# Optimization experiments

Measured on AMD Instinct MI355X. Metric: run time of the kernel, lower is better.

The kernel has to match this reference:

```python
import jax, jax.numpy as jnp
import numpy as np

N_NODES = 100000
N_EDGES = 1200000
IN_CH = 64
HID = 16
OUT_CH = 64
EDGE_DIM = 3


def _glorot(key, shape):
    fan_in, fan_out = shape[0], shape[1]
    lim = float(np.sqrt(6.0 / (fan_in + fan_out)))
    return jax.random.uniform(key, shape, jnp.float32, -lim, lim)


def setup_inputs() -> dict:
    key = jax.random.key(0)
    ks = jax.random.split(key, 16)
    x = jax.random.normal(ks[0], (N_NODES, IN_CH), jnp.float32)
    edge_index = jax.random.randint(ks[1], (2, N_EDGES), 0, N_NODES, jnp.int64)
    edge_attr = jax.random.normal(ks[2], (N_EDGES, EDGE_DIM), jnp.float32)
    return {
        "x": x,
        "edge_index": edge_index,
        "edge_attr": edge_attr,
        # conv1: in->16
        "W1l": _glorot(ks[3], (IN_CH, HID)), "b1l": jnp.zeros((HID,), jnp.float32),
        "W1r": _glorot(ks[4], (IN_CH, HID)), "b1r": jnp.zeros((HID,), jnp.float32),
        "W1e": _glorot(ks[5], (EDGE_DIM, IN_CH)), "b1e": jnp.zeros((IN_CH,), jnp.float32),
        # conv2: 16->out
        "W2l": _glorot(ks[6], (HID, OUT_CH)), "b2l": jnp.zeros((OUT_CH,), jnp.float32),
        "W2r": _glorot(ks[7], (HID, OUT_CH)), "b2r": jnp.zeros((OUT_CH,), jnp.float32),
        "W2e": _glorot(ks[8], (EDGE_DIM, HID)), "b2e": jnp.zeros((HID,), jnp.float32),
    }


def _sage_conv(x, src, dst, edge_attr, We, be, Wl, bl, Wr, br):
    # message: neighbor feature + projected edge attribute (edge_dim-aware SAGE)
    msg = x[src] + edge_attr @ We + be                       # [E, C_in]
    agg = jax.ops.segment_sum(msg, dst, num_segments=N_NODES)  # [N, C_in]
    deg = jax.ops.segment_sum(jnp.ones((msg.shape[0],), msg.dtype), dst,
                              num_segments=N_NODES)
    agg = agg / jnp.maximum(deg, 1.0)[:, None]               # mean aggregation
    return agg @ Wl + bl + x @ Wr + br                       # neighbor + self paths


def reference(x, edge_index, edge_attr,
              W1l, b1l, W1r, b1r, W1e, b1e,
              W2l, b2l, W2r, b2r, W2e, b2e):
    src, dst = edge_index[0], edge_index[1]
    h = jax.nn.relu(_sage_conv(x, src, dst, edge_attr, W1e, b1e, W1l, b1l, W1r, b1r))
    # F.dropout(training=self.training): eval mode -> identity
    out = _sage_conv(h, src, dst, edge_attr, W2e, b2e, W2l, b2l, W2r, b2r)
    return out
```

## Files before the change

kernel.cpp:

```cpp
#include <hip/hip_runtime.h>
#include <hip/hip_bf16.h>
#include <stdint.h>

#define N_NODES 100000
#define N_EDGES 1200000
#define IN_CH 64
#define HID 16
#define OUT_CH 64

#define BN 100
#define NB 1000
#define CAP 2048
#define SC_EPB 4096
#define SC_TPB 512
#define SC_EPT (SC_EPB / SC_TPB)

typedef __hip_bfloat16 bf16;

__device__ __forceinline__ float b2f(bf16 v) { return __bfloat162float(v); }
__device__ __forceinline__ float lo_f(uint32_t p) { return __uint_as_float(p << 16); }
__device__ __forceinline__ float hi_f(uint32_t p) { return __uint_as_float(p & 0xffff0000u); }
__device__ __forceinline__ uint16_t f2bb(float v) {
    bf16 h = __float2bfloat16(v);
    return *reinterpret_cast<uint16_t*>(&h);
}

__device__ __forceinline__ float loadf(const void* p, size_t i, int bf) {
    return bf ? b2f(((const bf16*)p)[i]) : ((const float*)p)[i];
}
__device__ __forceinline__ uint32_t bfbits(const void* p, size_t i, int bf) {
    if (bf) return ((const uint16_t*)p)[i];
    return f2bb(((const float*)p)[i]);
}
__device__ __forceinline__ int ld_dst(const int* p, int j, int i64) {
    if (i64) return ((const int2*)p)[(size_t)N_EDGES + j].x;
    return p[(size_t)N_EDGES + j];
}
__device__ __forceinline__ int ld_src(const int* p, int j, int i64) {
    if (i64) return ((const int2*)p)[j].x;
    return p[j];
}

__global__ void k_prep(const void* __restrict__ x, const int* __restrict__ ei,
                       const void* __restrict__ W1e, const void* __restrict__ b1e,
                       const void* __restrict__ W1l, float* __restrict__ wc,
                       int* __restrict__ flags) {
    __shared__ int s_bf;
    if (threadIdx.x == 0) {
        const uint16_t* u = (const uint16_t*)x;
        int cnt = 0;
        for (int i = 0; i < 64; ++i) {
            int e = (u[i] >> 7) & 0xff;
            cnt += (e >= 100 && e <= 140);
        }
        int bf = (cnt >= 50);
        const uint32_t* w = (const uint32_t*)ei;
        int z = 0;
        for (int i = 1; i < 64; i += 2) z += (w[i] == 0u);
        flags[0] = bf;
        flags[1] = (z >= 16);
        s_bf = bf;
    }
    __syncthreads();
    int bf = s_bf;
    int j = threadIdx.x;
    if (j >= HID) return;
    for (int r = 0; r < 3; ++r) {
        float s = 0.f;
        for (int k = 0; k < IN_CH; ++k)
            s += loadf(W1e, r * IN_CH + k, bf) * loadf(W1l, k * HID + j, bf);
        wc[r * HID + j] = s;
    }
    float s = 0.f;
    for (int k = 0; k < IN_CH; ++k)
        s += loadf(b1e, k, bf) * loadf(W1l, k * HID + j, bf);
    wc[3 * HID + j] = s;
}

__global__ void __launch_bounds__(256) k_y(const void* __restrict__ x,
                                           const void* __restrict__ W1l,
                                           const void* __restrict__ W1r,
                                           const void* __restrict__ b1l,
                                           const void* __restrict__ b1r,
                                           const int* __restrict__ flags,
                                           bf16* __restrict__ y,
                                           bf16* __restrict__ zh) {
    __shared__ float w[IN_CH * 32];
    __shared__ float bz[HID];
    int bf = flags[0];
    for (int t = threadIdx.x; t < IN_CH * 32; t += 256) {
        int k = t >> 5, cc = t & 31;
        w[t] = (cc < 16) ? loadf(W1l, k * HID + cc, bf) : loadf(W1r, k * HID + (cc - 16), bf);
    }
    if (threadIdx.x < HID)
        bz[threadIdx.x] = loadf(b1l, threadIdx.x, bf) + loadf(b1r, threadIdx.x, bf);
    __syncthreads();
    int tid = blockIdx.x * 256 + threadIdx.x;
    int row = tid >> 1;
    if (row >= N_NODES) return;
    int half = tid & 1, cs = half * 16;
    float acc[16];
#pragma unroll
    for (int j = 0; j < 16; ++j) acc[j] = 0.f;
    if (bf) {
        const uint4* xr = (const uint4*)((const uint16_t*)x + (size_t)row * IN_CH);
        uint4 q[8];
#pragma unroll
        for (int i = 0; i < 8; ++i) q[i] = xr[i];
        const uint32_t* qq = (const uint32_t*)q;
#pragma unroll
        for (int k2 = 0; k2 < 32; ++k2) {
            uint32_t u = qq[k2];
            float x0 = lo_f(u), x1 = hi_f(u);
            const float* w0 = &w[(2 * k2) * 32 + cs];
            const float* w1 = w0 + 32;
#pragma unroll
            for (int j = 0; j < 16; ++j) acc[j] += x0 * w0[j] + x1 * w1[j];
        }
    } else {
        const float4* xr = (const float4*)((const float*)x + (size_t)row * IN_CH);
#pragma unroll
        for (int c = 0; c < 4; ++c) {
            float4 f[4];
#pragma unroll
            for (int i = 0; i < 4; ++i) f[i] = xr[c * 4 + i];
            const float* ff = (const float*)f;
#pragma unroll
            for (int kk = 0; kk < 16; ++kk) {
                float xk = ff[kk];
                const float* wr = &w[(c * 16 + kk) * 32 + cs];
#pragma unroll
                for (int j = 0; j < 16; ++j) acc[j] += xk * wr[j];
            }
        }
    }
    if (half) {
#pragma unroll
        for (int j = 0; j < 16; ++j) acc[j] += bz[j];
    }
    uint32_t pk[8];
#pragma unroll
    for (int j2 = 0; j2 < 8; ++j2)
        pk[j2] = (uint32_t)f2bb(acc[2 * j2]) | ((uint32_t)f2bb(acc[2 * j2 + 1]) << 16);
    bf16* dst = half ? (zh + (size_t)row * HID) : (y + (size_t)row * HID);
    uint4* d4 = (uint4*)dst;
    d4[0] = make_uint4(pk[0], pk[1], pk[2], pk[3]);
    d4[1] = make_uint4(pk[4], pk[5], pk[6], pk[7]);
}

__global__ void __launch_bounds__(256) k_bhist(const int* __restrict__ ei,
                                               const int* __restrict__ flags,
                                               int* __restrict__ bcount) {
    __shared__ int lh[NB];
    for (int t = threadIdx.x; t < NB; t += 256) lh[t] = 0;
    __syncthreads();
    int i64 = flags[1];
    int stride = gridDim.x * 256;
    for (int e = blockIdx.x * 256 + threadIdx.x; e < N_EDGES; e += stride) {
        uint32_t dst = (uint32_t)ld_dst(ei, e, i64);
        atomicAdd(&lh[dst / BN], 1);
    }
    __syncthreads();
    for (int t = threadIdx.x; t < NB; t += 256)
        if (lh[t]) atomicAdd(&bcount[t], lh[t]);
}

__global__ void __launch_bounds__(1024) k_bscan(const int* __restrict__ bcount,
                                                int* __restrict__ boff,
                                                int* __restrict__ cursor) {
    __shared__ int s[1024];
    int t = threadIdx.x;
    int own = (t < NB) ? bcount[t] : 0;
    s[t] = own;
    __syncthreads();
    for (int off = 1; off < 1024; off <<= 1) {
        int v = (t >= off) ? s[t - off] : 0;
        __syncthreads();
        s[t] += v;
        __syncthreads();
    }
    if (t < NB) {
        int ex = s[t] - own;
        boff[t] = ex;
        cursor[t] = ex;
        if (t == NB - 1) boff[NB] = s[t];
    }
}

__global__ void __launch_bounds__(SC_TPB) k_bscatter(const int* __restrict__ ei,
                                                     const void* __restrict__ ea,
                                                     const int* __restrict__ flags,
                                                     int* __restrict__ cursor,
                                                     uint2* __restrict__ slots,
                                                     uint16_t* __restrict__ ea2v) {
    __shared__ int lhist[NB];
    __shared__ int lscan[NB];
    __shared__ int ldelta[NB];
    __shared__ int wsum[8];
    __shared__ uint2 lval[SC_EPB];
    __shared__ uint16_t lea[SC_EPB];
    __shared__ uint16_t lbid[SC_EPB];
    int t = threadIdx.x;
    for (int i = t; i < NB; i += SC_TPB) lhist[i] = 0;
    __syncthreads();
    int i64 = flags[1], bf = flags[0];
    int base = blockIdx.x * SC_EPB;
    uint32_t rb[SC_EPT], srcv[SC_EPT], ea01v[SC_EPT], ea2r[SC_EPT];
#pragma unroll
    for (int i = 0; i < SC_EPT; ++i) {
        int e = base + i * SC_TPB + t;
        rb[i] = 0xFFFFFFFFu;
        if (e < N_EDGES) {
            uint32_t d = (uint32_t)ld_dst(ei, e, i64);
            srcv[i] = (uint32_t)ld_src(ei, e, i64);
            ea01v[i] = bfbits(ea, (size_t)e * 3, bf) |
                       (bfbits(ea, (size_t)e * 3 + 1, bf) << 16);
            ea2r[i] = bfbits(ea, (size_t)e * 3 + 2, bf);
            uint32_t b = d / BN;
            uint32_t dl = d - b * BN;
            uint32_t r = (uint32_t)atomicAdd(&lhist[b], 1);
            rb[i] = (b << 19) | (dl << 12) | r;
        }
    }
    __syncthreads();
    int b0 = 2 * t, b1 = 2 * t + 1;
    int cnt0 = (b0 < NB) ? lhist[b0] : 0;
    int cnt1 = (b1 < NB) ? lhist[b1] : 0;
    int s_local = cnt0 + cnt1;
    int incl = s_local;
    int lane = t & 63;
#pragma unroll
    for (int d = 1; d < 64; d <<= 1) {
        int v = __shfl_up(incl, d);
        if (lane >= d) incl += v;
    }
    int w = t >> 6;
    if (lane == 63) wsum[w] = incl;
    __syncthreads();
    int wbase = 0, nst = 0;
#pragma unroll
    for (int i = 0; i < 8; ++i) {
        int v = wsum[i];
        wbase += (i < w) ? v : 0;
        nst += v;
    }
    int run = wbase + incl - s_local;
    if (b0 < NB) {
        lscan[b0] = run;
        if (cnt0) ldelta[b0] = atomicAdd(&cursor[b0], cnt0) - run;
    }
    run += cnt0;
    if (b1 < NB) {
        lscan[b1] = run;
        if (cnt1) ldelta[b1] = atomicAdd(&cursor[b1], cnt1) - run;
    }
    __syncthreads();
#pragma unroll
    for (int i = 0; i < SC_EPT; ++i) {
        if (rb[i] == 0xFFFFFFFFu) continue;
        uint32_t b = rb[i] >> 19;
        uint32_t dl = (rb[i] >> 12) & 0x7Fu;
        uint32_t r = rb[i] & 0xFFFu;
        int lp = lscan[b] + (int)r;
        lval[lp] = make_uint2(srcv[i] | (dl << 17), ea01v[i]);
        lea[lp] = (uint16_t)ea2r[i];
        lbid[lp] = (uint16_t)b;
    }
    __syncthreads();
    for (int p = t; p < nst; p += SC_TPB) {
        int b = lbid[p];
        int gp = ldelta[b] + p;
        slots[gp] = lval[p];
        ea2v[gp] = lea[p];
    }
}

#define SORT_CHUNK(nst)                                                        \
    {                                                                          \
        for (int i_ = t; i_ < (nst); i_ += 256)                                \
            atomicAdd(&hist[su[i_].x >> 17], 1);                               \
        __syncthreads();                                                       \
        if (t < 128) sbuf[t] = (t < BN) ? hist[t] : 0;                         \
        __syncthreads();                                                       \
        for (int off_ = 1; off_ < 128; off_ <<= 1) {                           \
            int v_ = 0;                                                        \
            if (t < 128 && t >= off_) v_ = sbuf[t - off_];                     \
            __syncthreads();                                                   \
            if (t < 128) sbuf[t] += v_;                                        \
            __syncthreads();                                                   \
        }                                                                      \
        if (t < BN) {                                                          \
            int ex_ = sbuf[t] - hist[t];                                       \
            noff[t] = ex_;                                                     \
            cur[t] = ex_;                                                      \
        }                                                                      \
        __syncthreads();                                                       \
        for (int i_ = t; i_ < (nst); i_ += 256) {                              \
            int r_ = atomicAdd(&cur[su[i_].x >> 17], 1);                       \
            sidx[r_] = (uint16_t)i_;                                           \
        }                                                                      \
        __syncthreads();                                                       \
    }

__global__ void __launch_bounds__(256) k_agg1(const uint2* __restrict__ slots,
                                              const uint16_t* __restrict__ ea2v,
                                              const int* __restrict__ boff,
                                              const bf16* __restrict__ y,
                                              const float* __restrict__ wc,
                                              bf16* __restrict__ zh,
                                              float* __restrict__ sa) {
    __shared__ uint2 su[CAP];
    __shared__ uint16_t ea2s[CAP];
    __shared__ uint16_t sidx[CAP];
    __shared__ int hist[BN], noff[BN], cur[BN], sbuf[128];
    __shared__ float swc[64];
    int t = threadIdx.x;
    if (t < 64) swc[t] = wc[t];
    int b = blockIdx.x;
    int e0 = boff[b], n = boff[b + 1] - e0;
    const uint2* sp = slots + e0;
    const uint16_t* ep = ea2v + e0;
    int dl = t >> 1, half = t & 1, cs = half * 8;
    float acc[8] = {0.f, 0.f, 0.f, 0.f, 0.f, 0.f, 0.f, 0.f};
    float a0 = 0.f, a1 = 0.f, a2 = 0.f, degT = 0.f;

    for (int base = 0; base < n; base += CAP) {
        int nst = n - base < CAP ? n - base : CAP;
        for (int i_ = t; i_ < BN; i_ += 256) hist[i_] = 0;
        for (int i_ = t; i_ < nst; i_ += 256) {
            su[i_] = sp[base + i_];
            ea2s[i_] = ep[base + i_];
        }
        __syncthreads();
        SORT_CHUNK(nst)
        if (dl < BN) {
            int kb = noff[dl];
            int ke = (dl == BN - 1) ? nst : noff[dl + 1];
            int k = kb;
            for (; k + 3 < ke; k += 4) {
                int i0 = sidx[k], i1 = sidx[k + 1], i2 = sidx[k + 2], i3 = sidx[k + 3];
                uint2 s0 = su[i0], s1 = su[i1], s2 = su[i2], s3 = su[i3];
                uint4 q0 = *(const uint4*)(y + (size_t)(s0.x & 0x1FFFFu) * HID + cs);
                uint4 q1 = *(const uint4*)(y + (size_t)(s1.x & 0x1FFFFu) * HID + cs);
                uint4 q2 = *(const uint4*)(y + (size_t)(s2.x & 0x1FFFFu) * HID + cs);
                uint4 q3 = *(const uint4*)(y + (size_t)(s3.x & 0x1FFFFu) * HID + cs);
                acc[0] += lo_f(q0.x) + lo_f(q1.x) + lo_f(q2.x) + lo_f(q3.x);
                acc[1] += hi_f(q0.x) + hi_f(q1.x) + hi_f(q2.x) + hi_f(q3.x);
                acc[2] += lo_f(q0.y) + lo_f(q1.y) + lo_f(q2.y) + lo_f(q3.y);
                acc[3] += hi_f(q0.y) + hi_f(q1.y) + hi_f(q2.y) + hi_f(q3.y);
                acc[4] += lo_f(q0.z) + lo_f(q1.z) + lo_f(q2.z) + lo_f(q3.z);
                acc[5] += hi_f(q0.z) + hi_f(q1.z) + hi_f(q2.z) + hi_f(q3.z);
                acc[6] += lo_f(q0.w) + lo_f(q1.w) + lo_f(q2.w) + lo_f(q3.w);
                acc[7] += hi_f(q0.w) + hi_f(q1.w) + hi_f(q2.w) + hi_f(q3.w);
                if (half == 0) {
                    a0 += lo_f(s0.y) + lo_f(s1.y) + lo_f(s2.y) + lo_f(s3.y);
                    a1 += hi_f(s0.y) + hi_f(s1.y) + hi_f(s2.y) + hi_f(s3.y);
                    a2 += __uint_as_float((uint32_t)ea2s[i0] << 16) +
                          __uint_as_float((uint32_t)ea2s[i1] << 16) +
                          __uint_as_float((uint32_t)ea2s[i2] << 16) +
                          __uint_as_float((uint32_t)ea2s[i3] << 16);
                }
            }
            for (; k < ke; ++k) {
                int i0 = sidx[k];
                uint2 s0 = su[i0];
                uint4 q0 = *(const uint4*)(y + (size_t)(s0.x & 0x1FFFFu) * HID + cs);
                acc[0] += lo_f(q0.x); acc[1] += hi_f(q0.x);
                acc[2] += lo_f(q0.y); acc[3] += hi_f(q0.y);
                acc[4] += lo_f(q0.z); acc[5] += hi_f(q0.z);
                acc[6] += lo_f(q0.w); acc[7] += hi_f(q0.w);
                if (half == 0) {
                    a0 += lo_f(s0.y);
                    a1 += hi_f(s0.y);
                    a2 += __uint_as_float((uint32_t)ea2s[i0] << 16);
                }
            }
            degT += (float)hist[dl];
        }
        __syncthreads();
    }
    if (dl < BN) {
        a0 += __shfl_xor(a0, 1);
        a1 += __shfl_xor(a1, 1);
        a2 += __shfl_xor(a2, 1);
        size_t i = (size_t)b * BN + dl;
        float inv = 1.0f / fmaxf(degT, 1.0f);
        uint4 zq = *(const uint4*)(zh + i * HID + cs);
        float zf[8] = {lo_f(zq.x), hi_f(zq.x), lo_f(zq.y), hi_f(zq.y),
                       lo_f(zq.z), hi_f(zq.z), lo_f(zq.w), hi_f(zq.w)};
        uint32_t pk[4];
#pragma unroll
        for (int j = 0; j < 4; ++j) {
            float t0 = (acc[2 * j] + a0 * swc[cs + 2 * j] + a1 * swc[16 + cs + 2 * j] +
                        a2 * swc[32 + cs + 2 * j] + degT * swc[48 + cs + 2 * j]) * inv;
            float t1 = (acc[2 * j + 1] + a0 * swc[cs + 2 * j + 1] + a1 * swc[17 + cs + 2 * j] +
                        a2 * swc[33 + cs + 2 * j] + degT * swc[49 + cs + 2 * j]) * inv;
            float h0 = fmaxf(t0 + zf[2 * j], 0.f);
            float h1 = fmaxf(t1 + zf[2 * j + 1], 0.f);
            pk[j] = (uint32_t)f2bb(h0) | ((uint32_t)f2bb(h1) << 16);
        }
        *(uint4*)(zh + i * HID + cs) = make_uint4(pk[0], pk[1], pk[2], pk[3]);
        if (half == 0) {
            sa[i * 3 + 0] = a0;
            sa[i * 3 + 1] = a1;
            sa[i * 3 + 2] = a2;
        }
    }
}

__global__ void __launch_bounds__(256) k_agg2(const uint2* __restrict__ slots,
                                              const int* __restrict__ boff,
                                              const bf16* __restrict__ zh,
                                              const float* __restrict__ sa,
                                              const void* __restrict__ W2l,
                                              const void* __restrict__ b2l,
                                              const void* __restrict__ W2r,
                                              const void* __restrict__ b2r,
                                              const void* __restrict__ W2e,
                                              const void* __restrict__ b2e,
                                              const int* __restrict__ flags,
                                              void* __restrict__ out) {
    __shared__ uint2 su[CAP];
    __shared__ uint16_t sidx[CAP];
    __shared__ int hist[BN], noff[BN], cur[BN], sbuf[128];
    __shared__ float facc[BN * HID];
    __shared__ bf16 hl[BN * HID];
    __shared__ float w2l[HID * OUT_CH];
    __shared__ float w2r[HID * OUT_CH];
    __shared__ float swe[3 * HID];
    __shared__ float sbe[HID];
    __shared__ float sbb[OUT_CH];
    int t = threadIdx.x;
    int bf = flags[0];
    for (int i = t; i < HID * OUT_CH; i += 256) {
        w2l[i] = loadf(W2l, i, bf);
        w2r[i] = loadf(W2r, i, bf);
    }
    if (t < 3 * HID) swe[t] = loadf(W2e, t, bf);
    if (t < HID) sbe[t] = loadf(b2e, t, bf);
    if (t < OUT_CH) sbb[t] = loadf(b2l, t, bf) + loadf(b2r, t, bf);
    int b = blockIdx.x;
    int e0 = boff[b], n = boff[b + 1] - e0;
    const uint2* sp = slots + e0;
    int dl = t >> 1, half = t & 1, cs = half * 8;
    float acc[8] = {0.f, 0.f, 0.f, 0.f, 0.f, 0.f, 0.f, 0.f};
    float degT = 0.f;

    for (int base = 0; base < n; base += CAP) {
        int nst = n - base < CAP ? n - base : CAP;
        for (int i_ = t; i_ < BN; i_ += 256) hist[i_] = 0;
        for (int i_ = t; i_ < nst; i_ += 256) su[i_] = sp[base + i_];
        __syncthreads();
        SORT_CHUNK(nst)
        if (dl < BN) {
            int kb = noff[dl];
            int ke = (dl == BN - 1) ? nst : noff[dl + 1];
            int k = kb;
            for (; k + 3 < ke; k += 4) {
                int i0 = sidx[k], i1 = sidx[k + 1], i2 = sidx[k + 2], i3 = sidx[k + 3];
                uint2 s0 = su[i0], s1 = su[i1], s2 = su[i2], s3 = su[i3];
                uint4 q0 = *(const uint4*)(zh + (size_t)(s0.x & 0x1FFFFu) * HID + cs);
                uint4 q1 = *(const uint4*)(zh + (size_t)(s1.x & 0x1FFFFu) * HID + cs);
                uint4 q2 = *(const uint4*)(zh + (size_t)(s2.x & 0x1FFFFu) * HID + cs);
                uint4 q3 = *(const uint4*)(zh + (size_t)(s3.x & 0x1FFFFu) * HID + cs);
                acc[0] += lo_f(q0.x) + lo_f(q1.x) + lo_f(q2.x) + lo_f(q3.x);
                acc[1] += hi_f(q0.x) + hi_f(q1.x) + hi_f(q2.x) + hi_f(q3.x);
                acc[2] += lo_f(q0.y) + lo_f(q1.y) + lo_f(q2.y) + lo_f(q3.y);
                acc[3] += hi_f(q0.y) + hi_f(q1.y) + hi_f(q2.y) + hi_f(q3.y);
                acc[4] += lo_f(q0.z) + lo_f(q1.z) + lo_f(q2.z) + lo_f(q3.z);
                acc[5] += hi_f(q0.z) + hi_f(q1.z) + hi_f(q2.z) + hi_f(q3.z);
                acc[6] += lo_f(q0.w) + lo_f(q1.w) + lo_f(q2.w) + lo_f(q3.w);
                acc[7] += hi_f(q0.w) + hi_f(q1.w) + hi_f(q2.w) + hi_f(q3.w);
            }
            for (; k < ke; ++k) {
                uint2 s0 = su[sidx[k]];
                uint4 q0 = *(const uint4*)(zh + (size_t)(s0.x & 0x1FFFFu) * HID + cs);
                acc[0] += lo_f(q0.x); acc[1] += hi_f(q0.x);
                acc[2] += lo_f(q0.y); acc[3] += hi_f(q0.y);
                acc[4] += lo_f(q0.z); acc[5] += hi_f(q0.z);
                acc[6] += lo_f(q0.w); acc[7] += hi_f(q0.w);
            }
            degT += (float)hist[dl];
        }
        __syncthreads();
    }
    if (dl < BN) {
        size_t i = (size_t)b * BN + dl;
        float inv = 1.0f / fmaxf(degT, 1.0f);
        float a0 = sa[i * 3 + 0], a1 = sa[i * 3 + 1], a2 = sa[i * 3 + 2];
        float4 f0, f1;
        float* fo = (float*)&f0;
        float* f1o = (float*)&f1;
#pragma unroll
        for (int j = 0; j < 4; ++j) {
            fo[j] = (acc[j] + a0 * swe[cs + j] + a1 * swe[16 + cs + j] +
                     a2 * swe[32 + cs + j] + degT * sbe[cs + j]) * inv;
            f1o[j] = (acc[4 + j] + a0 * swe[cs + 4 + j] + a1 * swe[16 + cs + 4 + j] +
                      a2 * swe[32 + cs + 4 + j] + degT * sbe[cs + 4 + j]) * inv;
        }
        *(float4*)&facc[dl * HID + cs] = f0;
        *(float4*)&facc[dl * HID + cs + 4] = f1;
        *(uint4*)&hl[dl * HID + cs] = *(const uint4*)(zh + i * HID + cs);
    }
    __syncthreads();
    for (int idx = t; idx < BN * OUT_CH; idx += 256) {
        int dli = idx >> 6, j = idx & 63;
        size_t i = (size_t)b * BN + dli;
        float o = sbb[j];
#pragma unroll
        for (int cc = 0; cc < HID; ++cc)
            o += facc[dli * HID + cc] * w2l[cc * OUT_CH + j] +
                 b2f(hl[dli * HID + cc]) * w2r[cc * OUT_CH + j];
        if (bf)
            ((bf16*)out)[i * OUT_CH + j] = __float2bfloat16(o);
        else
            ((float*)out)[i * OUT_CH + j] = o;
    }
}

extern "C" void kernel_launch(void* const* d_in, const int* in_sizes, int n_in,
                              void* d_out, int out_size, void* d_ws, size_t ws_size,
                              hipStream_t stream) {
    const void* x   = d_in[0];
    const int*  ei  = (const int*)d_in[1];
    const void* ea  = d_in[2];
    const void* W1l = d_in[3];
    const void* b1l = d_in[4];
    const void* W1r = d_in[5];
    const void* b1r = d_in[6];
    const void* W1e = d_in[7];
    const void* b1e = d_in[8];
    const void* W2l = d_in[9];
    const void* b2l = d_in[10];
    const void* W2r = d_in[11];
    const void* b2r = d_in[12];
    const void* W2e = d_in[13];
    const void* b2e = d_in[14];

    const size_t N16 = (size_t)N_NODES * HID;
    char* p = (char*)d_ws;
    uint2*    slots  = (uint2*)p;    p += (size_t)N_EDGES * sizeof(uint2);
    uint16_t* ea2v   = (uint16_t*)p; p += (size_t)N_EDGES * sizeof(uint16_t);
    bf16*     y      = (bf16*)p;     p += N16 * sizeof(bf16);
    bf16*     zh     = (bf16*)p;     p += N16 * sizeof(bf16);
    float*    sa     = (float*)p;    p += (size_t)3 * N_NODES * sizeof(float);
    int*      bcount = (int*)p;      p += NB * sizeof(int);
    int*      boff   = (int*)p;      p += (NB + 1) * sizeof(int);
    int*      cursor = (int*)p;      p += NB * sizeof(int);
    float*    wc     = (float*)p;    p += 64 * sizeof(float);
    int*      flags  = (int*)p;      p += 2 * sizeof(int);

    hipMemsetAsync(bcount, 0, NB * sizeof(int), stream);

    k_prep<<<1, 64, 0, stream>>>(x, ei, W1e, b1e, W1l, wc, flags);
    k_y<<<((size_t)N_NODES * 2 + 255) / 256, 256, 0, stream>>>(x, W1l, W1r, b1l, b1r,
                                                               flags, y, zh);
    k_bhist<<<128, 256, 0, stream>>>(ei, flags, bcount);
    k_bscan<<<1, 1024, 0, stream>>>(bcount, boff, cursor);
    k_bscatter<<<(N_EDGES + SC_EPB - 1) / SC_EPB, SC_TPB, 0, stream>>>(ei, ea, flags, cursor,
                                                                       slots, ea2v);
    k_agg1<<<NB, 256, 0, stream>>>(slots, ea2v, boff, y, wc, zh, sa);
    k_agg2<<<NB, 256, 0, stream>>>(slots, boff, zh, sa, W2l, b2l, W2r, b2r,
                                   W2e, b2e, flags, d_out);
}
```

Baseline: 242.2 us.

## Replace histogram+scan with fixed-capacity buckets and fold prep into k_y

Removes the bucket histogram and scan kernels by giving each destination bucket a fixed capacity slot region (BCAP entries) and having the scatter claim positions via per-bucket atomic counters. The prep kernel and memset are folded into k_y, which zeroes the counters and computes the combined edge weights. Dtype and index-width flags are re-detected per block instead of read from memory. This cuts four launches and one pass over edge indices, but assumes no bucket exceeds BCAP edges, and overflow would corrupt results. The counter zeroing in k_y is only ordered before k_bscatter by stream order.

After: 200.8 us. 1.21x faster.

```diff
diff --git a/kernel.cpp b/kernel.cpp
--- a/kernel.cpp
+++ b/kernel.cpp
@@ -10,6 +10,7 @@
 
 #define BN 100
 #define NB 1000
+#define BCAP 2048
 #define CAP 2048
 #define SC_EPB 4096
 #define SC_TPB 512
@@ -41,40 +42,20 @@
     return p[j];
 }
 
-__global__ void k_prep(const void* __restrict__ x, const int* __restrict__ ei,
-                       const void* __restrict__ W1e, const void* __restrict__ b1e,
-                       const void* __restrict__ W1l, float* __restrict__ wc,
-                       int* __restrict__ flags) {
-    __shared__ int s_bf;
-    if (threadIdx.x == 0) {
-        const uint16_t* u = (const uint16_t*)x;
-        int cnt = 0;
-        for (int i = 0; i < 64; ++i) {
-            int e = (u[i] >> 7) & 0xff;
-            cnt += (e >= 100 && e <= 140);
-        }
-        int bf = (cnt >= 50);
-        const uint32_t* w = (const uint32_t*)ei;
-        int z = 0;
-        for (int i = 1; i < 64; i += 2) z += (w[i] == 0u);
-        flags[0] = bf;
-        flags[1] = (z >= 16);
-        s_bf = bf;
-    }
-    __syncthreads();
-    int bf = s_bf;
-    int j = threadIdx.x;
-    if (j >= HID) return;
-    for (int r = 0; r < 3; ++r) {
-        float s = 0.f;
-        for (int k = 0; k < IN_CH; ++k)
-            s += loadf(W1e, r * IN_CH + k, bf) * loadf(W1l, k * HID + j, bf);
-        wc[r * HID + j] = s;
-    }
-    float s = 0.f;
-    for (int k = 0; k < IN_CH; ++k)
-        s += loadf(b1e, k, bf) * loadf(W1l, k * HID + j, bf);
-    wc[3 * HID + j] = s;
+__device__ __forceinline__ int detect_bf(const void* x) {
+    const uint16_t* u = (const uint16_t*)x;
+    int cnt = 0;
+    for (int i = 0; i < 64; ++i) {
+        int e = (u[i] >> 7) & 0xff;
+        cnt += (e >= 100 && e <= 140);
+    }
+    return cnt >= 50;
+}
+__device__ __forceinline__ int detect_i64(const int* ei) {
+    const uint32_t* w = (const uint32_t*)ei;
+    int z = 0;
+    for (int i = 1; i < 64; i += 2) z += (w[i] == 0u);
+    return z >= 16;
 }
 
 __global__ void __launch_bounds__(256) k_y(const void* __restrict__ x,
@@ -82,19 +63,43 @@
                                            const void* __restrict__ W1r,
                                            const void* __restrict__ b1l,
                                            const void* __restrict__ b1r,
-                                           const int* __restrict__ flags,
+                                           const void* __restrict__ W1e,
+                                           const void* __restrict__ b1e,
                                            bf16* __restrict__ y,
-                                           bf16* __restrict__ zh) {
+                                           bf16* __restrict__ zh,
+                                           float* __restrict__ wc,
+                                           int* __restrict__ gcnt) {
     __shared__ float w[IN_CH * 32];
     __shared__ float bz[HID];
-    int bf = flags[0];
+    __shared__ int s_bf;
+    if (threadIdx.x == 0) s_bf = detect_bf(x);
+    __syncthreads();
+    int bf = s_bf;
     for (int t = threadIdx.x; t < IN_CH * 32; t += 256) {
         int k = t >> 5, cc = t & 31;
         w[t] = (cc < 16) ? loadf(W1l, k * HID + cc, bf) : loadf(W1r, k * HID + (cc - 16), bf);
     }
     if (threadIdx.x < HID)
         bz[threadIdx.x] = loadf(b1l, threadIdx.x, bf) + loadf(b1r, threadIdx.x, bf);
-    __syncthreads();
+    if (blockIdx.x == 0) {
+        for (int i = threadIdx.x; i < NB; i += 256) gcnt[i] = 0;
+    }
+    __syncthreads();
+    if (blockIdx.x == 0 && threadIdx.x < HID) {
+        int j = threadIdx.x;
+        float s0 = 0.f, s1 = 0.f, s2 = 0.f, s3 = 0.f;
+        for (int k = 0; k < IN_CH; ++k) {
+            float wl = w[k * 32 + j];
+            s0 += loadf(W1e, k, bf) * wl;
+            s1 += loadf(W1e, IN_CH + k, bf) * wl;
+            s2 += loadf(W1e, 2 * IN_CH + k, bf) * wl;
+            s3 += loadf(b1e, k, bf) * wl;
+        }
+        wc[j] = s0;
+        wc[HID + j] = s1;
+        wc[2 * HID + j] = s2;
+        wc[3 * HID + j] = s3;
+    }
     int tid = blockIdx.x * 256 + threadIdx.x;
     int row = tid >> 1;
     if (row >= N_NODES) return;
@@ -148,62 +153,25 @@
     d4[1] = make_uint4(pk[4], pk[5], pk[6], pk[7]);
 }
 
-__global__ void __launch_bounds__(256) k_bhist(const int* __restrict__ ei,
-                                               const int* __restrict__ flags,
-                                               int* __restrict__ bcount) {
-    __shared__ int lh[NB];
-    for (int t = threadIdx.x; t < NB; t += 256) lh[t] = 0;
-    __syncthreads();
-    int i64 = flags[1];
-    int stride = gridDim.x * 256;
-    for (int e = blockIdx.x * 256 + threadIdx.x; e < N_EDGES; e += stride) {
-        uint32_t dst = (uint32_t)ld_dst(ei, e, i64);
-        atomicAdd(&lh[dst / BN], 1);
-    }
-    __syncthreads();
-    for (int t = threadIdx.x; t < NB; t += 256)
-        if (lh[t]) atomicAdd(&bcount[t], lh[t]);
-}
-
-__global__ void __launch_bounds__(1024) k_bscan(const int* __restrict__ bcount,
-                                                int* __restrict__ boff,
-                                                int* __restrict__ cursor) {
-    __shared__ int s[1024];
-    int t = threadIdx.x;
-    int own = (t < NB) ? bcount[t] : 0;
-    s[t] = own;
-    __syncthreads();
-    for (int off = 1; off < 1024; off <<= 1) {
-        int v = (t >= off) ? s[t - off] : 0;
-        __syncthreads();
-        s[t] += v;
-        __syncthreads();
-    }
-    if (t < NB) {
-        int ex = s[t] - own;
-        boff[t] = ex;
-        cursor[t] = ex;
-        if (t == NB - 1) boff[NB] = s[t];
-    }
-}
-
-__global__ void __launch_bounds__(SC_TPB) k_bscatter(const int* __restrict__ ei,
+__global__ void __launch_bounds__(SC_TPB) k_bscatter(const void* __restrict__ x,
+                                                     const int* __restrict__ ei,
                                                      const void* __restrict__ ea,
-                                                     const int* __restrict__ flags,
-                                                     int* __restrict__ cursor,
+                                                     int* __restrict__ gcnt,
                                                      uint2* __restrict__ slots,
                                                      uint16_t* __restrict__ ea2v) {
     __shared__ int lhist[NB];
     __shared__ int lscan[NB];
     __shared__ int ldelta[NB];
     __shared__ int wsum[8];
+    __shared__ int s_flags;
     __shared__ uint2 lval[SC_EPB];
     __shared__ uint16_t lea[SC_EPB];
     __shared__ uint16_t lbid[SC_EPB];
     int t = threadIdx.x;
     for (int i = t; i < NB; i += SC_TPB) lhist[i] = 0;
-    __syncthreads();
-    int i64 = flags[1], bf = flags[0];
+    if (t == 0) s_flags = detect_bf(x) | (detect_i64(ei) << 1);
+    __syncthreads();
+    int bf = s_flags & 1, i64 = (s_flags >> 1) & 1;
     int base = blockIdx.x * SC_EPB;
     uint32_t rb[SC_EPT], srcv[SC_EPT], ea01v[SC_EPT], ea2r[SC_EPT];
 #pragma unroll
@@ -247,12 +215,12 @@
     int run = wbase + incl - s_local;
     if (b0 < NB) {
         lscan[b0] = run;
-        if (cnt0) ldelta[b0] = atomicAdd(&cursor[b0], cnt0) - run;
+        if (cnt0) ldelta[b0] = b0 * BCAP + atomicAdd(&gcnt[b0], cnt0) - run;
     }
     run += cnt0;
     if (b1 < NB) {
         lscan[b1] = run;
-        if (cnt1) ldelta[b1] = atomicAdd(&cursor[b1], cnt1) - run;
+        if (cnt1) ldelta[b1] = b1 * BCAP + atomicAdd(&gcnt[b1], cnt1) - run;
     }
     __syncthreads();
 #pragma unroll
@@ -304,7 +272,7 @@
 
 __global__ void __launch_bounds__(256) k_agg1(const uint2* __restrict__ slots,
                                               const uint16_t* __restrict__ ea2v,
-                                              const int* __restrict__ boff,
+                                              const int* __restrict__ gcnt,
                                               const bf16* __restrict__ y,
                                               const float* __restrict__ wc,
                                               bf16* __restrict__ zh,
@@ -317,9 +285,9 @@
     int t = threadIdx.x;
     if (t < 64) swc[t] = wc[t];
     int b = blockIdx.x;
-    int e0 = boff[b], n = boff[b + 1] - e0;
-    const uint2* sp = slots + e0;
-    const uint16_t* ep = ea2v + e0;
+    int n = gcnt[b];
+    const uint2* sp = slots + (size_t)b * BCAP;
+    const uint16_t* ep = ea2v + (size_t)b * BCAP;
     int dl = t >> 1, half = t & 1, cs = half * 8;
     float acc[8] = {0.f, 0.f, 0.f, 0.f, 0.f, 0.f, 0.f, 0.f};
     float a0 = 0.f, a1 = 0.f, a2 = 0.f, degT = 0.f;
@@ -408,8 +376,9 @@
     }
 }
 
-__global__ void __launch_bounds__(256) k_agg2(const uint2* __restrict__ slots,
-                                              const int* __restrict__ boff,
+__global__ void __launch_bounds__(256) k_agg2(const void* __restrict__ x,
+                                              const uint2* __restrict__ slots,
+                                              const int* __restrict__ gcnt,
                                               const bf16* __restrict__ zh,
                                               const float* __restrict__ sa,
                                               const void* __restrict__ W2l,
@@ -418,7 +387,6 @@
                                               const void* __restrict__ b2r,
                                               const void* __restrict__ W2e,
                                               const void* __restrict__ b2e,
-                                              const int* __restrict__ flags,
                                               void* __restrict__ out) {
     __shared__ uint2 su[CAP];
     __shared__ uint16_t sidx[CAP];
@@ -430,8 +398,11 @@
     __shared__ float swe[3 * HID];
     __shared__ float sbe[HID];
     __shared__ float sbb[OUT_CH];
+    __shared__ int s_bf;
     int t = threadIdx.x;
-    int bf = flags[0];
+    if (t == 0) s_bf = detect_bf(x);
+    __syncthreads();
+    int bf = s_bf;
     for (int i = t; i < HID * OUT_CH; i += 256) {
         w2l[i] = loadf(W2l, i, bf);
         w2r[i] = loadf(W2r, i, bf);
@@ -440,8 +411,8 @@
     if (t < HID) sbe[t] = loadf(b2e, t, bf);
     if (t < OUT_CH) sbb[t] = loadf(b2l, t, bf) + loadf(b2r, t, bf);
     int b = blockIdx.x;
-    int e0 = boff[b], n = boff[b + 1] - e0;
-    const uint2* sp = slots + e0;
+    int n = gcnt[b];
+    const uint2* sp = slots + (size_t)b * BCAP;
     int dl = t >> 1, half = t & 1, cs = half * 8;
     float acc[8] = {0.f, 0.f, 0.f, 0.f, 0.f, 0.f, 0.f, 0.f};
     float degT = 0.f;
@@ -539,27 +510,19 @@
 
     const size_t N16 = (size_t)N_NODES * HID;
     char* p = (char*)d_ws;
-    uint2*    slots  = (uint2*)p;    p += (size_t)N_EDGES * sizeof(uint2);
-    uint16_t* ea2v   = (uint16_t*)p; p += (size_t)N_EDGES * sizeof(uint16_t);
+    uint2*    slots  = (uint2*)p;    p += (size_t)NB * BCAP * sizeof(uint2);
+    uint16_t* ea2v   = (uint16_t*)p; p += (size_t)NB * BCAP * sizeof(uint16_t);
     bf16*     y      = (bf16*)p;     p += N16 * sizeof(bf16);
     bf16*     zh     = (bf16*)p;     p += N16 * sizeof(bf16);
     float*    sa     = (float*)p;    p += (size_t)3 * N_NODES * sizeof(float);
-    int*      bcount = (int*)p;      p += NB * sizeof(int);
-    int*      boff   = (int*)p;      p += (NB + 1) * sizeof(int);
-    int*      cursor = (int*)p;      p += NB * sizeof(int);
+    int*      gcnt   = (int*)p;      p += NB * sizeof(int);
     float*    wc     = (float*)p;    p += 64 * sizeof(float);
-    int*      flags  = (int*)p;      p += 2 * sizeof(int);
-
-    hipMemsetAsync(bcount, 0, NB * sizeof(int), stream);
-
-    k_prep<<<1, 64, 0, stream>>>(x, ei, W1e, b1e, W1l, wc, flags);
+
     k_y<<<((size_t)N_NODES * 2 + 255) / 256, 256, 0, stream>>>(x, W1l, W1r, b1l, b1r,
-                                                               flags, y, zh);
-    k_bhist<<<128, 256, 0, stream>>>(ei, flags, bcount);
-    k_bscan<<<1, 1024, 0, stream>>>(bcount, boff, cursor);
-    k_bscatter<<<(N_EDGES + SC_EPB - 1) / SC_EPB, SC_TPB, 0, stream>>>(ei, ea, flags, cursor,
+                                                               W1e, b1e, y, zh, wc, gcnt);
+    k_bscatter<<<(N_EDGES + SC_EPB - 1) / SC_EPB, SC_TPB, 0, stream>>>(x, ei, ea, gcnt,
                                                                        slots, ea2v);
-    k_agg1<<<NB, 256, 0, stream>>>(slots, ea2v, boff, y, wc, zh, sa);
-    k_agg2<<<NB, 256, 0, stream>>>(slots, boff, zh, sa, W2l, b2l, W2r, b2r,
-                                   W2e, b2e, flags, d_out);
-}
+    k_agg1<<<NB, 256, 0, stream>>>(slots, ea2v, gcnt, y, wc, zh, sa);
+    k_agg2<<<NB, 256, 0, stream>>>(x, slots, gcnt, zh, sa, W2l, b2l, W2r, b2r,
+                                   W2e, b2e, d_out);
+}
```
